# Kernel optimization log

Hardware: AMD Instinct MI355X
Metric: run time of the kernel (lower is better)

The kernel has to match this reference:

```python
import jax, jax.numpy as jnp
import numpy as np
from jax import lax

CONF_THRES = 0.25
IOU_THRES = 0.45
MAX_WH = 4096.0   # class offset, agnostic=False
MAX_DET = 300
NEG = jnp.float32(-1e30)


def setup_inputs() -> dict:
    key = jax.random.key(0)
    B, N, C = 16, 25200, 85  # 640x640 yolov5, nc=80
    k1, k2, k3, k4 = jax.random.split(key, 4)
    xy = jax.random.uniform(k1, (B, N, 2), jnp.float32, 0.0, 640.0)
    wh = jax.random.uniform(k2, (B, N, 2), jnp.float32, 4.0, 120.0)
    obj = jax.random.uniform(k3, (B, N, 1), jnp.float32)
    cls = jax.random.uniform(k4, (B, N, C - 5), jnp.float32)
    prediction = jnp.concatenate([xy, wh, obj, cls], axis=-1)
    return {"prediction": prediction}


def _xywh2xyxy(b):
    # b: [N,4] (cx,cy,w,h) -> (x1,y1,x2,y2)
    return jnp.concatenate([b[:, :2] - b[:, 2:4] * 0.5,
                            b[:, :2] + b[:, 2:4] * 0.5], axis=1)


def _iou_one_vs_all(box, boxes):
    # box: [4], boxes: [N,4], plain IoU as in torchvision.ops.nms
    x1 = jnp.maximum(box[0], boxes[:, 0])
    y1 = jnp.maximum(box[1], boxes[:, 1])
    x2 = jnp.minimum(box[2], boxes[:, 2])
    y2 = jnp.minimum(box[3], boxes[:, 3])
    inter = jnp.clip(x2 - x1, 0.0) * jnp.clip(y2 - y1, 0.0)
    a1 = (box[2] - box[0]) * (box[3] - box[1])
    a2 = (boxes[:, 2] - boxes[:, 0]) * (boxes[:, 3] - boxes[:, 1])
    return inter / (a1 + a2 - inter)


def _nms_image(p):
    # p: [N, 5+nc] single-image predictions (decoded xywh, obj, class scores)
    obj = p[:, 4]                               # [N]
    cls_scores = p[:, 5:] * obj[:, None]        # x[:,5:] *= x[:,4:5]
    conf = jnp.max(cls_scores, axis=1)          # best-class conf
    j = jnp.argmax(cls_scores, axis=1)          # best class id
    boxes = _xywh2xyxy(p[:, :4])                # [N,4]
    valid = (obj > CONF_THRES) & (conf > CONF_THRES)
    # class-offset boxes for per-class NMS (agnostic=False)
    nms_boxes = boxes + (j.astype(boxes.dtype) * MAX_WH)[:, None]

    s0 = jnp.where(valid, conf, NEG)

    def step(s_live, _):
        i = jnp.argmax(s_live)
        sel = s_live[i]
        keep = sel > 0.0
        iou = _iou_one_vs_all(nms_boxes[i], nms_boxes)
        suppress = keep & (iou > IOU_THRES)
        s_new = jnp.where(suppress, NEG, s_live).at[i].set(NEG)
        return s_new, (i, keep)

    _, (idxs, keeps) = lax.scan(step, s0, None, length=MAX_DET)
    # output rows [x1,y1,x2,y2,conf,cls] — boxes WITHOUT class offset
    rows = jnp.concatenate([boxes[idxs], conf[idxs, None],
                            j[idxs, None].astype(boxes.dtype)], axis=1)
    rows = rows * keeps[:, None].astype(rows.dtype)  # zero padded slots
    return rows, keeps


def reference(prediction):
    # prediction: [B, N, 5+nc] -> ([B, MAX_DET, 6], [B, MAX_DET] keep mask)
    out, keep = jax.vmap(_nms_image)(prediction)
    return out, keep
```

## Files before the change

### kernel.cpp

```cpp
#include <hip/hip_runtime.h>
#include <cstdint>
#include <cfloat>

#define BATCH 16
#define NBOX 25200
#define CH 85
#define NCLS 80
#define CAP 512
#define SEGCAP 128
#define ACC 32
#define MAXDET 300
#define RPB 112
#define CNTPAD 16

typedef unsigned long long u64;

__device__ __forceinline__ u64 shflx64(u64 v, int m) {
    int lo = __shfl_xor((int)(unsigned)(v & 0xffffffffu), m);
    int hi = __shfl_xor((int)(unsigned)(v >> 32), m);
    return ((u64)(unsigned)hi << 32) | (u64)(unsigned)lo;
}

__global__ __launch_bounds__(256) void pre_kernel(const float* __restrict__ p,
                                                  int* __restrict__ cnt,
                                                  u64* __restrict__ rec,
                                                  float* __restrict__ outZero,
                                                  int outN) {
#pragma clang fp contract(off)
    __shared__ float s[RPB * CH];
    int tid = threadIdx.x;

    long z = (long)blockIdx.x * 256 + tid;
    if (z < outN) outZero[z] = 0.0f;

    long blockRow = (long)blockIdx.x * RPB;

    const float4* p4 = (const float4*)(p + blockRow * CH);
    float4* s4 = (float4*)s;
    for (int t = tid; t < RPB * CH / 4; t += 256) {
        __builtin_amdgcn_global_load_lds(
            (const __attribute__((address_space(1))) void*)(p4 + t),
            (__attribute__((address_space(3))) void*)(s4 + (t & ~63)),
            16, 0, 0);
    }
    __syncthreads();

    int r = tid >> 1;
    int half = tid & 1;
    if (r < RPB) {
        const float* row = s + r * CH;
        float obj = row[4];

        float v = -FLT_MAX; int c = 1000;
        int c0 = half * 40;
        for (int k = 0; k < 40; k++) {
            float sc = row[5 + c0 + k] * obj;
            int cc = c0 + k;
            if (sc > v) { v = sc; c = cc; }
        }
        float v2 = __shfl_xor(v, 1);
        int   cz = __shfl_xor(c, 1);
        if (v2 > v || (v2 == v && cz < c)) { v = v2; c = cz; }

        if (half == 0 && obj > 0.25f && v > 0.25f) {
            int wid = (int)blockRow + r;
            int b   = wid / NBOX;
            int idx = wid - b * NBOX;
            u64 key = ((u64)__float_as_uint(v) << 22) | ((u64)(32767 - idx) << 7) | (u64)c;
            int bkt = b * NCLS + c;
            int seg = idx & 3;
            int pos = atomicAdd(&cnt[bkt * CNTPAD + seg], 1);
            if (pos < SEGCAP) {
                float x = row[0], y = row[1], w = row[2], h = row[3];
                float hw = w * 0.5f, hh = h * 0.5f;
                float offc = (float)c * 4096.0f;
                float4 b4;
                b4.x = (x - hw) + offc; b4.y = (y - hh) + offc;
                b4.z = (x + hw) + offc; b4.w = (y + hh) + offc;
                u64* slot = rec + ((long)bkt * CAP + seg * SEGCAP + pos) * 4;
                *(float4*)slot = b4;
                slot[2] = key;
            }
        }
    }
}

__global__ __launch_bounds__(64) void nms_kernel(const int* __restrict__ cnt,
                                                 const u64* __restrict__ rec,
                                                 u64* __restrict__ accKey) {
#pragma clang fp contract(off)
    __shared__ float4 posBox[CAP];
    __shared__ u64    posKeyS[CAP];
    int lane = threadIdx.x;
    int bkt = blockIdx.x;

    const int* cb = cnt + bkt * CNTPAD;
    int ns[4];
#pragma unroll
    for (int s2 = 0; s2 < 4; s2++) {
        int v = cb[s2];
        ns[s2] = (v < SEGCAP) ? v : SEGCAP;
    }

    const u64* R = rec + (long)bkt * CAP * 4;
    u64 key[8];
#pragma unroll
    for (int r = 0; r < 8; r++) {
        int slot = (r << 6) | lane;
        float4 b4 = *(const float4*)(R + (long)slot * 4);
        u64 k = R[(long)slot * 4 + 2];
        posBox[slot] = b4;
        int off = ((r & 1) << 6) | lane;
        key[r] = (off < ns[r >> 1]) ? ((k << 9) | (u64)slot) : 0ULL;
    }
    __syncthreads();

#define CE_XL(K, LM)                                                    \
    { bool d = ((lane & ((K) >> 3)) == 0);                              \
      _Pragma("unroll")                                                 \
      for (int r = 0; r < 8; r++) {                                     \
          u64 part = shflx64(key[r], (LM));                             \
          bool up = ((lane & (LM)) == 0);                               \
          bool gt = key[r] > part;                                      \
          u64 mx = gt ? key[r] : part;                                  \
          u64 mn = gt ? part : key[r];                                  \
          key[r] = (d == up) ? mx : mn; } }
#define CE_RR(K, M)                                                    \
    { _Pragma("unroll")                                                \
      for (int r = 0; r < 8; r++) if (!(r & (M))) {                    \
          int r2 = r | (M);                                            \
          u64 a = key[r], e = key[r2];                                 \
          bool d = ((r & (K)) == 0);                                   \
          u64 hi = (a > e) ? a : e, lo = (a > e) ? e : a;              \
          key[r]  = d ? hi : lo;                                       \
          key[r2] = d ? lo : hi; } }
#define CE_RL(K, M)                                                    \
    { bool d = ((lane & ((K) >> 3)) == 0);                             \
      _Pragma("unroll")                                                \
      for (int r = 0; r < 8; r++) if (!(r & (M))) {                    \
          int r2 = r | (M);                                            \
          u64 a = key[r], e = key[r2];                                 \
          u64 hi = (a > e) ? a : e, lo = (a > e) ? e : a;              \
          key[r]  = d ? hi : lo;                                       \
          key[r2] = d ? lo : hi; } }

    CE_RR(2, 1)
    CE_RR(4, 2) CE_RR(4, 1)
    CE_RL(8, 4) CE_RL(8, 2) CE_RL(8, 1)
    CE_XL(16, 1)  CE_RL(16, 4)  CE_RL(16, 2)  CE_RL(16, 1)
    CE_XL(32, 2)  CE_XL(32, 1)  CE_RL(32, 4)  CE_RL(32, 2)  CE_RL(32, 1)
    CE_XL(64, 4)  CE_XL(64, 2)  CE_XL(64, 1)  CE_RL(64, 4)  CE_RL(64, 2)  CE_RL(64, 1)
    CE_XL(128, 8) CE_XL(128, 4) CE_XL(128, 2) CE_XL(128, 1)
    CE_RL(128, 4) CE_RL(128, 2) CE_RL(128, 1)
    CE_XL(256, 16) CE_XL(256, 8) CE_XL(256, 4) CE_XL(256, 2) CE_XL(256, 1)
    CE_RL(256, 4)  CE_RL(256, 2) CE_RL(256, 1)
    CE_XL(512, 32) CE_XL(512, 16) CE_XL(512, 8) CE_XL(512, 4) CE_XL(512, 2) CE_XL(512, 1)
    CE_RL(512, 4)  CE_RL(512, 2)  CE_RL(512, 1)
#undef CE_XL
#undef CE_RR
#undef CE_RL

    float x1[8], y1[8], x2[8], y2[8], ar[8];
    unsigned live = 0;
#pragma unroll
    for (int r = 0; r < 8; r++) {
        int slot = (int)(key[r] & 511u);
        float4 B = posBox[slot];
        x1[r] = B.x; y1[r] = B.y; x2[r] = B.z; y2[r] = B.w;
        ar[r] = (B.z - B.x) * (B.w - B.y);
        if (key[r] != 0ULL) live |= 1u << r;
    }
    __syncthreads();

#pragma unroll
    for (int r = 0; r < 8; r++) {
        int t = (r << 6) | lane;
        posBox[t]  = make_float4(x1[r], y1[r], x2[r], y2[r]);
        posKeyS[t] = key[r] >> 9;
    }
    __syncthreads();

    long obase = (long)bkt * ACC;
    int nacc = 0;
    u64 mask = __ballot(live != 0);
    while (mask != 0ULL) {
        int L = (int)__ffsll((long long)mask) - 1;
        unsigned lv = (unsigned)__builtin_amdgcn_readlane((int)live, L);
        int r0 = __ffs((int)lv) - 1;
        int tp = (r0 << 6) | L;
        float4 B = posBox[tp];
        u64 kk = posKeyS[tp];
        if (lane == 0) accKey[obase + nacc] = kk;
        nacc++;
        if (lane == L) live &= ~(1u << r0);
        if (nacc == ACC) break;
        float A = (B.z - B.x) * (B.w - B.y);
#pragma unroll
        for (int r = 0; r < 8; r++) {
            if ((live >> r) & 1) {
                float xx1 = fmaxf(B.x, x1[r]);
                float yy1 = fmaxf(B.y, y1[r]);
                float xx2 = fminf(B.z, x2[r]);
                float yy2 = fminf(B.w, y2[r]);
                float inter = fmaxf(xx2 - xx1, 0.0f) * fmaxf(yy2 - yy1, 0.0f);
                float uni = (A + ar[r]) - inter;
                if (inter / uni > 0.45f) live &= ~(1u << r);
            }
        }
        mask = __ballot(live != 0);
    }
    for (int t2 = nacc + lane; t2 < ACC; t2 += 64) accKey[obase + t2] = 0ULL;
}

__global__ __launch_bounds__(256) void merge_kernel(const float* __restrict__ p,
                                                    const u64* __restrict__ accKey,
                                                    float* __restrict__ outRows,
                                                    float* __restrict__ outKeep) {
#pragma clang fp contract(off)
    __shared__ u64 L[NCLS * ACC];
    int tid = threadIdx.x;
    int b = blockIdx.y;
    const u64* src = accKey + (long)b * NCLS * ACC;
    for (int t = tid; t < NCLS * ACC; t += 256) L[t] = src[t];
    __syncthreads();

    int g = blockIdx.x * 256 + tid;
    u64 key = L[g];
    if (key == 0ULL) return;
    int cOwn = g / ACC;
    int rank = g - cOwn * ACC;

    int d = 1;
    for (; d + 3 < NCLS; d += 4) {
        int ca = cOwn + d;     if (ca >= NCLS) ca -= NCLS;
        int cb = cOwn + d + 1; if (cb >= NCLS) cb -= NCLS;
        int cc = cOwn + d + 2; if (cc >= NCLS) cc -= NCLS;
        int cd = cOwn + d + 3; if (cd >= NCLS) cd -= NCLS;
        const u64* LA = L + ca * ACC;
        const u64* LB = L + cb * ACC;
        const u64* LC = L + cc * ACC;
        const u64* LD = L + cd * ACC;
        int na = 0, nb = 0, nc = 0, nd = 0;
#pragma unroll
        for (int s2 = 32; s2; s2 >>= 1) {
            int ta = na + s2, tb = nb + s2, tc = nc + s2, td = nd + s2;
            if (ta <= ACC && LA[ta - 1] > key) na = ta;
            if (tb <= ACC && LB[tb - 1] > key) nb = tb;
            if (tc <= ACC && LC[tc - 1] > key) nc = tc;
            if (td <= ACC && LD[td - 1] > key) nd = td;
        }
        rank += na + nb + nc + nd;
        if (rank >= MAXDET) return;
    }
    for (; d < NCLS; d++) {
        int c2 = cOwn + d; if (c2 >= NCLS) c2 -= NCLS;
        const u64* Lc = L + c2 * ACC;
        int cn = 0;
#pragma unroll
        for (int s2 = 32; s2; s2 >>= 1) {
            int ncx = cn + s2;
            if (ncx <= ACC && Lc[ncx - 1] > key) cn = ncx;
        }
        rank += cn;
        if (rank >= MAXDET) return;
    }

    int cc  = (int)(key & 127);
    int idx = 32767 - (int)((key >> 7) & 32767);
    float conf = __uint_as_float((unsigned)(key >> 22));
    const float* q = p + ((long)b * NBOX + idx) * CH;
    float x = q[0], y = q[1], w = q[2], h = q[3];
    float hw = w * 0.5f, hh = h * 0.5f;
    float* row = outRows + ((long)b * MAXDET + rank) * 6;
    row[0] = x - hw; row[1] = y - hh; row[2] = x + hw; row[3] = y + hh;
    row[4] = conf;   row[5] = (float)cc;
    outKeep[b * MAXDET + rank] = 1.0f;
}

extern "C" void kernel_launch(void* const* d_in, const int* in_sizes, int n_in,
                              void* d_out, int out_size, void* d_ws, size_t ws_size,
                              hipStream_t stream) {
    const float* p = (const float*)d_in[0];
    float* out = (float*)d_out;

    char* ws = (char*)d_ws;
    int* cnt = (int*)ws;
    u64* rec = (u64*)(ws + BATCH * NCLS * CNTPAD * 4);
    u64* accKey = (u64*)(ws + BATCH * NCLS * CNTPAD * 4
                            + (size_t)BATCH * NCLS * CAP * 32);

    hipMemsetAsync(cnt, 0, BATCH * NCLS * CNTPAD * sizeof(int), stream);
    pre_kernel<<<(BATCH * NBOX) / RPB, 256, 0, stream>>>(p, cnt, rec, out, out_size);
    nms_kernel<<<BATCH * NCLS, 64, 0, stream>>>(cnt, rec, accKey);
    dim3 gM(NCLS * ACC / 256, BATCH);
    merge_kernel<<<gM, 256, 0, stream>>>(p, accKey, out, out + (size_t)BATCH * MAXDET * 6);
}
```

Baseline: 278.9 us.

## Replace serial greedy NMS loop with tiled 64x64 IoU bitmask suppression

Per-class NMS no longer runs a serial loop that picks one box and does a ballot for each pick. It now processes the sorted candidates in tiles of 64. Each lane builds a 64-bit suppression row against the other boxes in its tile and first checks its box against boxes already accepted from earlier tiles. The greedy pick is then resolved with wave-uniform bitmask operations on the shared rows. This trades the serial latency for more redundant IoU work (63 divisions per lane per tile) and an extra barrier per tile.

```diff
diff --git a/kernel.cpp b/kernel.cpp
--- a/kernel.cpp
+++ b/kernel.cpp
@@ -91,16 +91,19 @@
 #pragma clang fp contract(off)
     __shared__ float4 posBox[CAP];
     __shared__ u64    posKeyS[CAP];
+    __shared__ u64    rowLds[64];
+    __shared__ int    pickPosLds[ACC];
     int lane = threadIdx.x;
     int bkt = blockIdx.x;
 
     const int* cb = cnt + bkt * CNTPAD;
-    int ns[4];
-#pragma unroll
-    for (int s2 = 0; s2 < 4; s2++) {
-        int v = cb[s2];
-        ns[s2] = (v < SEGCAP) ? v : SEGCAP;
-    }
+    int ns0 = cb[0], ns1 = cb[1], ns2 = cb[2], ns3 = cb[3];
+    ns0 = ns0 < SEGCAP ? ns0 : SEGCAP;
+    ns1 = ns1 < SEGCAP ? ns1 : SEGCAP;
+    ns2 = ns2 < SEGCAP ? ns2 : SEGCAP;
+    ns3 = ns3 < SEGCAP ? ns3 : SEGCAP;
+    int nsg[4] = {ns0, ns1, ns2, ns3};
+    int ntot = ns0 + ns1 + ns2 + ns3;
 
     const u64* R = rec + (long)bkt * CAP * 4;
     u64 key[8];
@@ -111,7 +114,7 @@
         u64 k = R[(long)slot * 4 + 2];
         posBox[slot] = b4;
         int off = ((r & 1) << 6) | lane;
-        key[r] = (off < ns[r >> 1]) ? ((k << 9) | (u64)slot) : 0ULL;
+        key[r] = (off < nsg[r >> 1]) ? ((k << 9) | (u64)slot) : 0ULL;
     }
     __syncthreads();
 
@@ -160,55 +163,79 @@
 #undef CE_RR
 #undef CE_RL
 
-    float x1[8], y1[8], x2[8], y2[8], ar[8];
-    unsigned live = 0;
+    float4 pb[8]; u64 pk[8];
 #pragma unroll
     for (int r = 0; r < 8; r++) {
         int slot = (int)(key[r] & 511u);
-        float4 B = posBox[slot];
-        x1[r] = B.x; y1[r] = B.y; x2[r] = B.z; y2[r] = B.w;
-        ar[r] = (B.z - B.x) * (B.w - B.y);
-        if (key[r] != 0ULL) live |= 1u << r;
-    }
-    __syncthreads();
-
+        pb[r] = posBox[slot];
+        pk[r] = key[r] >> 9;
+    }
+    __syncthreads();
 #pragma unroll
     for (int r = 0; r < 8; r++) {
-        int t = (r << 6) | lane;
-        posBox[t]  = make_float4(x1[r], y1[r], x2[r], y2[r]);
-        posKeyS[t] = key[r] >> 9;
+        int t = (lane << 3) | r;
+        posBox[t]  = pb[r];
+        posKeyS[t] = pk[r];
     }
     __syncthreads();
 
     long obase = (long)bkt * ACC;
     int nacc = 0;
-    u64 mask = __ballot(live != 0);
-    while (mask != 0ULL) {
-        int L = (int)__ffsll((long long)mask) - 1;
-        unsigned lv = (unsigned)__builtin_amdgcn_readlane((int)live, L);
-        int r0 = __ffs((int)lv) - 1;
-        int tp = (r0 << 6) | L;
-        float4 B = posBox[tp];
-        u64 kk = posKeyS[tp];
-        if (lane == 0) accKey[obase + nacc] = kk;
-        nacc++;
-        if (lane == L) live &= ~(1u << r0);
-        if (nacc == ACC) break;
-        float A = (B.z - B.x) * (B.w - B.y);
-#pragma unroll
-        for (int r = 0; r < 8; r++) {
-            if ((live >> r) & 1) {
-                float xx1 = fmaxf(B.x, x1[r]);
-                float yy1 = fmaxf(B.y, y1[r]);
-                float xx2 = fminf(B.z, x2[r]);
-                float yy2 = fminf(B.w, y2[r]);
+    for (int tb = 0; tb < CAP; tb += 64) {
+        if (tb >= ntot || nacc >= ACC) break;
+        if (tb > 0) __syncthreads();
+
+        bool valid = (tb + lane) < ntot;
+        float4 my = posBox[tb + lane];
+        float myA = (my.z - my.x) * (my.w - my.y);
+        bool dead = !valid;
+
+        if (tb > 0) {
+            for (int k = 0; k < nacc; k++) {
+                float4 B = posBox[pickPosLds[k]];
+                float xx1 = fmaxf(B.x, my.x);
+                float yy1 = fmaxf(B.y, my.y);
+                float xx2 = fminf(B.z, my.z);
+                float yy2 = fminf(B.w, my.w);
                 float inter = fmaxf(xx2 - xx1, 0.0f) * fmaxf(yy2 - yy1, 0.0f);
-                float uni = (A + ar[r]) - inter;
-                if (inter / uni > 0.45f) live &= ~(1u << r);
+                float A = (B.z - B.x) * (B.w - B.y);
+                float uni = (A + myA) - inter;
+                if (valid && (inter / uni > 0.45f)) dead = true;
             }
         }
-        mask = __ballot(live != 0);
-    }
+
+        u64 row = 0;
+#pragma unroll 4
+        for (int k = 1; k < 64; k++) {
+            int j = (lane + k) & 63;
+            float4 B = posBox[tb + j];
+            float xx1 = fmaxf(my.x, B.x);
+            float yy1 = fmaxf(my.y, B.y);
+            float xx2 = fminf(my.z, B.z);
+            float yy2 = fminf(my.w, B.w);
+            float inter = fmaxf(xx2 - xx1, 0.0f) * fmaxf(yy2 - yy1, 0.0f);
+            float aj = (B.z - B.x) * (B.w - B.y);
+            float uni = (myA + aj) - inter;
+            if (inter / uni > 0.45f) row |= 1ULL << j;
+        }
+
+        u64 alive = __ballot(!dead);
+        rowLds[lane] = row;
+        __syncthreads();
+
+        while (alive != 0ULL && nacc < ACC) {
+            int pos = (int)__ffsll((long long)alive) - 1;
+            if (lane == 0) {
+                accKey[obase + nacc] = posKeyS[tb + pos];
+                pickPosLds[nacc] = tb + pos;
+            }
+            nacc++;
+            u64 krow = rowLds[pos];
+            alive &= ~krow;
+            alive &= ~(1ULL << pos);
+        }
+    }
+
     for (int t2 = nacc + lane; t2 < ACC; t2 += 64) accKey[obase + t2] = 0ULL;
 }
 
@@ -243,9 +270,9 @@
         int na = 0, nb = 0, nc = 0, nd = 0;
 #pragma unroll
         for (int s2 = 32; s2; s2 >>= 1) {
-            int ta = na + s2, tb = nb + s2, tc = nc + s2, td = nd + s2;
+            int ta = na + s2, tb2 = nb + s2, tc = nc + s2, td = nd + s2;
             if (ta <= ACC && LA[ta - 1] > key) na = ta;
-            if (tb <= ACC && LB[tb - 1] > key) nb = tb;
+            if (tb2 <= ACC && LB[tb2 - 1] > key) nb = tb2;
             if (tc <= ACC && LC[tc - 1] > key) nc = tc;
             if (td <= ACC && LD[td - 1] > key) nd = td;
         }
```

New measurement: 262.8 us. -5.8%, faster.
